# Optimization experiments

Hardware: AMD Instinct MI355X
Metric: run time of the kernel (lower is better)

Reference implementation:

```python
import jax, jax.numpy as jnp
import numpy as np

B, N, D, V = 512, 200, 128, 100000

def setup_inputs() -> dict:
    key = jax.random.key(0)
    ks = jax.random.split(key, 13)
    s = 1.0 / np.sqrt(D)
    return {
        "x": jax.random.randint(ks[0], (B, N), 0, V),
        "A": jax.random.uniform(ks[1], (B, N, 2 * N), dtype=jnp.float32),
        "emb": jax.random.normal(ks[2], (V, D), dtype=jnp.float32) * s,
        "w_in": jax.random.normal(ks[3], (D, D), dtype=jnp.float32) * s,
        "b_in": jax.random.normal(ks[4], (D,), dtype=jnp.float32) * s,
        "w_out": jax.random.normal(ks[5], (D, D), dtype=jnp.float32) * s,
        "b_out": jax.random.normal(ks[6], (D,), dtype=jnp.float32) * s,
        "w_ih": jax.random.normal(ks[7], (3 * D, 2 * D), dtype=jnp.float32) * s,
        "b_ih": jax.random.normal(ks[8], (3 * D,), dtype=jnp.float32) * s,
        "w_hh": jax.random.normal(ks[9], (3 * D, D), dtype=jnp.float32) * s,
        "b_hh": jax.random.normal(ks[10], (3 * D,), dtype=jnp.float32) * s,
        "b_iah": jax.random.normal(ks[11], (D,), dtype=jnp.float32) * s,
        "b_oah": jax.random.normal(ks[12], (D,), dtype=jnp.float32) * s,
    }

def reference(x, A, emb, w_in, b_in, w_out, b_out, w_ih, b_ih, w_hh, b_hh, b_iah, b_oah):
    hidden = emb[x]                                   # [B, N, D]
    n = A.shape[1]
    # neighbor aggregation via in/out adjacency halves
    input_in = jnp.matmul(A[:, :, :n], hidden @ w_in.T + b_in) + b_iah    # [B, N, D]
    input_out = jnp.matmul(A[:, :, n:2 * n], hidden @ w_out.T + b_out) + b_oah
    inputs = jnp.concatenate([input_in, input_out], axis=2)               # [B, N, 2D]
    gi = inputs @ w_ih.T + b_ih                        # [B, N, 3D]
    gh = hidden @ w_hh.T + b_hh                        # [B, N, 3D]
    d = hidden.shape[-1]
    i_r, i_i, i_n = gi[..., :d], gi[..., d:2 * d], gi[..., 2 * d:]
    h_r, h_i, h_n = gh[..., :d], gh[..., d:2 * d], gh[..., 2 * d:]
    gate_input = jax.nn.sigmoid(i_i + h_i)
    gate_reset = jax.nn.sigmoid(i_r + h_r)
    gate_output = jnp.tanh(i_n + gate_reset * h_n)
    return gate_output + gate_input * (hidden - gate_output)
```

## Files before the change

### kernel.cpp

```cpp
#include <hip/hip_runtime.h>
#include <math.h>

#define BB 512
#define NN 200
#define DD 128
#define BNROWS (BB*NN)

typedef float f32x4 __attribute__((ext_vector_type(4)));
typedef short bf16x8 __attribute__((ext_vector_type(8)));

#define MFMA16(a,b,c) __builtin_amdgcn_mfma_f32_16x16x32_bf16(a,b,c,0,0,0)

#define GLL(gp, lp) __builtin_amdgcn_global_load_lds( \
    (const __attribute__((address_space(1))) unsigned int*)(gp), \
    (__attribute__((address_space(3))) unsigned int*)(lp), 16, 0, 0)

#define OFF_ZHI   ((size_t)0)
#define OFF_ZLO   (OFF_ZHI + (size_t)BNROWS*384*2)
#define OFF_HT    (OFF_ZLO + (size_t)BNROWS*256*2)
#define OFF_M1    (OFF_HT  + (size_t)BB*128*224*2)
#define OFF_M2    (OFF_M1  + (size_t)384*128*4)
#define OFF_WH    (OFF_M2  + (size_t)384*128*4)
#define OFF_WL    (OFF_WH  + (size_t)512*384*2)
#define OFF_CC    (OFF_WL  + (size_t)512*384*2)
#define OFF_U1V   (OFF_CC  + 512*4)
#define OFF_U2V   (OFF_U1V + 512*4)
#define OFF_U1    (OFF_U2V + 512*4)
#define OFF_U2    (OFF_U1  + 384*4)
#define OFF_C0    (OFF_U2  + 384*4)
#define OFF_RSI   (OFF_C0  + 384*4)
#define OFF_RSO   (OFF_RSI + (size_t)BNROWS*4)
#define WS_BYTES  (OFF_RSO + (size_t)BNROWS*4)

__device__ inline unsigned short f2bf(float x) {
  unsigned int u = __float_as_uint(x);
  unsigned int r = u + 0x7FFFu + ((u >> 16) & 1u);
  return (unsigned short)(r >> 16);
}
__device__ inline float bf2f(unsigned short h) {
  return __uint_as_float(((unsigned int)h) << 16);
}
__device__ inline float fsigmoid(float x) {
  return 1.f / (1.f + __expf(-x));
}
__device__ inline float ftanh(float x) {
  x = fminf(15.f, fmaxf(-15.f, x));
  float e = __expf(-2.f * x);
  return (1.f - e) / (1.f + e);
}

__global__ __launch_bounds__(128) void kprep(
    const float* __restrict__ w_ih, const float* __restrict__ w_in,
    const float* __restrict__ w_out, const float* __restrict__ b_in,
    const float* __restrict__ b_out, const float* __restrict__ b_iah,
    const float* __restrict__ b_oah, const float* __restrict__ b_ih,
    float* __restrict__ M1, float* __restrict__ M2,
    float* __restrict__ u1, float* __restrict__ u2, float* __restrict__ c0) {
  __shared__ float wrow[256];
  const int j = blockIdx.x;
  const int k = threadIdx.x;
  wrow[k]       = w_ih[(size_t)j * 256 + k];
  wrow[128 + k] = w_ih[(size_t)j * 256 + 128 + k];
  __syncthreads();
  float a1 = 0.f, a2 = 0.f;
  for (int t = 0; t < 128; ++t) {
    a1 = fmaf(wrow[t],       w_in[t * 128 + k],  a1);
    a2 = fmaf(wrow[128 + t], w_out[t * 128 + k], a2);
  }
  M1[j * 128 + k] = a1;
  M2[j * 128 + k] = a2;
  if (k == 0) {
    float s1 = 0.f, s2 = 0.f, s0 = 0.f;
    for (int t = 0; t < 128; ++t) {
      s1 = fmaf(wrow[t], b_in[t], s1);
      s2 = fmaf(wrow[128 + t], b_out[t], s2);
      s0 = fmaf(wrow[t], b_iah[t], s0);
      s0 = fmaf(wrow[128 + t], b_oah[t], s0);
    }
    u1[j] = s1; u2[j] = s2; c0[j] = s0 + b_ih[j];
  }
}

__global__ void wcat_build(const float* __restrict__ M1, const float* __restrict__ M2,
                           const float* __restrict__ w_hh, const float* __restrict__ b_hh,
                           const float* __restrict__ u1, const float* __restrict__ u2,
                           const float* __restrict__ c0,
                           unsigned short* __restrict__ Wh, unsigned short* __restrict__ Wl,
                           float* __restrict__ cc, float* __restrict__ u1v,
                           float* __restrict__ u2v) {
  int idx = blockIdx.x * 256 + threadIdx.x;
  if (idx >= 512 * 384) return;
  int jp = idx / 384, k = idx - jp * 384;
  int nh = jp >> 8, ng = (jp >> 7) & 1, t = (jp >> 4) & 7, q = jp & 15;
  int blk = t >> 1, s = t & 1;
  int c = nh * 64 + ng * 32 + s * 16 + q;
  int g = (blk <= 1) ? blk : 2;
  int j = g * 128 + c;
  float val;
  if (k < 128)      val = (blk == 3) ? 0.f : M1[j * 128 + k];
  else if (k < 256) val = (blk == 3) ? 0.f : M2[j * 128 + (k - 128)];
  else              val = (blk == 2) ? 0.f : w_hh[(size_t)j * 128 + (k - 256)];
  unsigned short h = f2bf(val);
  Wh[idx] = h;
  Wl[idx] = f2bf(val - bf2f(h));
  if (k == 0) {
    float ccv, a1, a2;
    if (blk == 0)      { ccv = c0[c] + b_hh[c];             a1 = u1[c];       a2 = u2[c]; }
    else if (blk == 1) { ccv = c0[128 + c] + b_hh[128 + c]; a1 = u1[128 + c]; a2 = u2[128 + c]; }
    else if (blk == 2) { ccv = c0[256 + c];                 a1 = u1[256 + c]; a2 = u2[256 + c]; }
    else               { ccv = b_hh[256 + c];               a1 = 0.f;         a2 = 0.f; }
    cc[jp] = ccv; u1v[jp] = a1; u2v[jp] = a2;
  }
}

__global__ __launch_bounds__(256) void k1_gather(
    const int* __restrict__ x, const float* __restrict__ emb,
    unsigned short* __restrict__ hT, unsigned short* __restrict__ Z_hi) {
  __shared__ float hid[32][132];
  const int t = threadIdx.x;
  const int b = blockIdx.x;
  const int m0 = blockIdx.y * 32;
  for (int i = t; i < 32 * 128; i += 256) {
    int r = i >> 7, c = i & 127;
    int m = m0 + r;
    int rowc = b * 200 + (m < 200 ? m : 199);
    float h = emb[(size_t)x[rowc] * 128 + c];
    hid[r][c] = h;
    if (m < 200) Z_hi[(size_t)(b * 200 + m) * 384 + 256 + c] = f2bf(h);
  }
  __syncthreads();
  {
    int c = t >> 1, half = t & 1;
    bf16x8 p0, p1;
    #pragma unroll
    for (int j = 0; j < 16; ++j) {
      int ml = half * 16 + j;
      bool valid = (m0 + ml) < 200;
      float fv = valid ? hid[ml][c] : 0.f;
      if (j < 8) p0[j] = (short)f2bf(fv);
      else       p1[j - 8] = (short)f2bf(fv);
    }
    size_t base = ((size_t)(b * 128 + c)) * 224 + m0 + half * 16;
    *(bf16x8*)&hT[base]     = p0;
    *(bf16x8*)&hT[base + 8] = p1;
  }
}

__global__ __launch_bounds__(256) void k2_amm(
    const float* __restrict__ A, const unsigned short* __restrict__ hT,
    unsigned short* __restrict__ Z_hi, unsigned short* __restrict__ Z_lo,
    float* __restrict__ rs_in, float* __restrict__ rs_out) {
  __shared__ alignas(16) unsigned short Ainh[64][32];
  __shared__ alignas(16) unsigned short Ainl[64][32];
  __shared__ alignas(16) unsigned short Aouth[64][32];
  __shared__ alignas(16) unsigned short Aoutl[64][32];
  __shared__ alignas(16) unsigned short Bv[128][32];
  const int t = threadIdx.x;
  const int b = blockIdx.x;
  const int m0 = blockIdx.y * 64;
  const int wv_id = t >> 6, lane = t & 63;
  const int q = lane & 15, quad = lane >> 4;
  const int sel = wv_id >> 1, nh2 = wv_id & 1;
  f32x4 acc[4][4];
  #pragma unroll
  for (int i = 0; i < 4; ++i)
    #pragma unroll
    for (int j = 0; j < 4; ++j) acc[i][j] = 0.f;
  float rsi = 0.f, rso = 0.f;

  for (int k0 = 0; k0 < 224; k0 += 32) {
    __syncthreads();
    {
      int m = t >> 2, seg = t & 3;
      int gm = m0 + m, kb = k0 + seg * 8;
      float fin[8], fot[8];
      bool v = (gm < 200) && (kb < 200);
      if (v) {
        const float* arow = A + (size_t)(b * 200 + gm) * 400;
        f32x4 p0 = *(const f32x4*)(arow + kb);
        f32x4 p1 = *(const f32x4*)(arow + kb + 4);
        f32x4 q0 = *(const f32x4*)(arow + 200 + kb);
        f32x4 q1 = *(const f32x4*)(arow + 200 + kb + 4);
        fin[0]=p0.x; fin[1]=p0.y; fin[2]=p0.z; fin[3]=p0.w;
        fin[4]=p1.x; fin[5]=p1.y; fin[6]=p1.z; fin[7]=p1.w;
        fot[0]=q0.x; fot[1]=q0.y; fot[2]=q0.z; fot[3]=q0.w;
        fot[4]=q1.x; fot[5]=q1.y; fot[6]=q1.z; fot[7]=q1.w;
      } else {
        #pragma unroll
        for (int e = 0; e < 8; ++e) { fin[e] = 0.f; fot[e] = 0.f; }
      }
      bf16x8 ih, il, oh, ol;
      #pragma unroll
      for (int e = 0; e < 8; ++e) {
        rsi += fin[e]; rso += fot[e];
        unsigned short h1 = f2bf(fin[e]);
        ih[e] = (short)h1; il[e] = (short)f2bf(fin[e] - bf2f(h1));
        unsigned short h2 = f2bf(fot[e]);
        oh[e] = (short)h2; ol[e] = (short)f2bf(fot[e] - bf2f(h2));
      }
      *(bf16x8*)&Ainh[m][seg * 8]  = ih;
      *(bf16x8*)&Ainl[m][seg * 8]  = il;
      *(bf16x8*)&Aouth[m][seg * 8] = oh;
      *(bf16x8*)&Aoutl[m][seg * 8] = ol;
    }
    #pragma unroll
    for (int p = 0; p < 2; ++p) {
      int i = p * 256 + t;
      int c = i >> 2, seg = i & 3;
      size_t off = ((size_t)(b * 128 + c)) * 224 + k0 + seg * 8;
      *(bf16x8*)&Bv[c][seg * 8] = *(const bf16x8*)(hT + off);
    }
    __syncthreads();
    const unsigned short (*Ath)[32] = sel ? Aouth : Ainh;
    const unsigned short (*Atl)[32] = sel ? Aoutl : Ainl;
    bf16x8 ah[4], al[4];
    #pragma unroll
    for (int mt = 0; mt < 4; ++mt) {
      ah[mt] = *(const bf16x8*)&Ath[mt * 16 + q][quad * 8];
      al[mt] = *(const bf16x8*)&Atl[mt * 16 + q][quad * 8];
    }
    #pragma unroll
    for (int nt = 0; nt < 4; ++nt) {
      bf16x8 bb = *(const bf16x8*)&Bv[nh2 * 64 + nt * 16 + q][quad * 8];
      #pragma unroll
      for (int mt = 0; mt < 4; ++mt) {
        acc[mt][nt] = MFMA16(ah[mt], bb, acc[mt][nt]);
        acc[mt][nt] = MFMA16(al[mt], bb, acc[mt][nt]);
      }
    }
  }
  const int colbase = sel * 128;
  #pragma unroll
  for (int nt = 0; nt < 4; ++nt) {
    int c = nh2 * 64 + nt * 16 + q;
    #pragma unroll
    for (int mt = 0; mt < 4; ++mt) {
      #pragma unroll
      for (int r = 0; r < 4; ++r) {
        int m = m0 + mt * 16 + quad * 4 + r;
        if (m < 200) {
          float v = acc[mt][nt][r];
          unsigned short hs = f2bf(v);
          size_t row = (size_t)(b * 200 + m);
          Z_hi[row * 384 + colbase + c] = hs;
          Z_lo[row * 256 + colbase + c] = f2bf(v - bf2f(hs));
        }
      }
    }
  }
  rsi += __shfl_xor(rsi, 1); rsi += __shfl_xor(rsi, 2);
  rso += __shfl_xor(rso, 1); rso += __shfl_xor(rso, 2);
  {
    int m = t >> 2, gm = m0 + m;
    if ((t & 3) == 0 && gm < 200) {
      rs_in[(size_t)b * 200 + gm]  = rsi;
      rs_out[(size_t)b * 200 + gm] = rso;
    }
  }
}

__global__ __launch_bounds__(256, 2) void k3_gates(
    const unsigned short* __restrict__ Z_hi, const unsigned short* __restrict__ Z_lo,
    const unsigned short* __restrict__ Wh, const unsigned short* __restrict__ Wl,
    const float* __restrict__ cc, const float* __restrict__ u1v,
    const float* __restrict__ u2v, const float* __restrict__ rs_in,
    const float* __restrict__ rs_out, float* __restrict__ out) {
  __shared__ alignas(16) unsigned short WhS[256][32];
  __shared__ alignas(16) unsigned short WlS[256][32];
  __shared__ alignas(16) unsigned short Ah[2][128][32];
  __shared__ alignas(16) unsigned short Al[2][128][32];
  const int t = threadIdx.x;
  const int w = t >> 6, lane = t & 63;
  const int q = lane & 15, quad = lane >> 4;
  const int mh = w >> 1, ng = w & 1;
  const int lrow = lane >> 2, lseg = lane & 3;
  const size_t rbase = (size_t)blockIdx.x * 128;
  const int nh = blockIdx.y;

  f32x4 acc[4][8];
  #pragma unroll
  for (int i = 0; i < 4; ++i)
    #pragma unroll
    for (int j = 0; j < 8; ++j) acc[i][j] = 0.f;

  #define STAGE_W(KC) do {                                                      \
    const int k0_ = (KC) * 32;                                                  \
    _Pragma("unroll")                                                           \
    for (int c_ = 0; c_ < 4; ++c_) {                                            \
      int j_ = w * 64 + c_ * 16;                                                \
      GLL(Wh + (size_t)(nh * 256 + j_ + lrow) * 384 + k0_ + lseg * 8,           \
          &WhS[j_][0]);                                                         \
    }                                                                           \
    _Pragma("unroll")                                                           \
    for (int c_ = 0; c_ < 4; ++c_) {                                            \
      int j_ = w * 64 + c_ * 16;                                                \
      GLL(Wl + (size_t)(nh * 256 + j_ + lrow) * 384 + k0_ + lseg * 8,           \
          &WlS[j_][0]);                                                         \
    }                                                                           \
  } while (0)

  #define STAGE_A1(KC, BUF) do {                                                \
    const int k0_ = (KC) * 32;                                                  \
    _Pragma("unroll")                                                           \
    for (int c_ = 0; c_ < 2; ++c_) {                                            \
      int m_ = w * 32 + c_ * 16;                                                \
      GLL(Z_hi + (rbase + m_ + lrow) * 384 + k0_ + lseg * 8, &Ah[BUF][m_][0]);  \
    }                                                                           \
    _Pragma("unroll")                                                           \
    for (int c_ = 0; c_ < 2; ++c_) {                                            \
      int m_ = w * 32 + c_ * 16;                                                \
      GLL(Z_lo + (rbase + m_ + lrow) * 256 + k0_ + lseg * 8, &Al[BUF][m_][0]);  \
    }                                                                           \
  } while (0)

  #define STAGE_A2(KC, BUF) do {                                                \
    const int k0_ = (KC) * 32;                                                  \
    _Pragma("unroll")                                                           \
    for (int c_ = 0; c_ < 2; ++c_) {                                            \
      int m_ = w * 32 + c_ * 16;                                                \
      GLL(Z_hi + (rbase + m_ + lrow) * 384 + k0_ + lseg * 8, &Ah[BUF][m_][0]);  \
    }                                                                           \
  } while (0)

  #define COMPUTE1(BUF) do {                                                    \
    bf16x8 ah_[4], al_[4];                                                      \
    _Pragma("unroll")                                                           \
    for (int mt = 0; mt < 4; ++mt) {                                            \
      ah_[mt] = *(const bf16x8*)&Ah[BUF][mh * 64 + mt * 16 + q][quad * 8];      \
      al_[mt] = *(const bf16x8*)&Al[BUF][mh * 64 + mt * 16 + q][quad * 8];      \
    }                                                                           \
    _Pragma("unroll")                                                           \
    for (int tt = 0; tt < 6; ++tt) {                                            \
      bf16x8 bh = *(const bf16x8*)&WhS[ng * 128 + tt * 16 + q][quad * 8];       \
      bf16x8 bl = *(const bf16x8*)&WlS[ng * 128 + tt * 16 + q][quad * 8];       \
      _Pragma("unroll")                                                         \
      for (int mt = 0; mt < 4; ++mt) {                                          \
        acc[mt][tt] = MFMA16(ah_[mt], bh, acc[mt][tt]);                         \
        acc[mt][tt] = MFMA16(ah_[mt], bl, acc[mt][tt]);                         \
        acc[mt][tt] = MFMA16(al_[mt], bh, acc[mt][tt]);                         \
      }                                                                         \
    }                                                                           \
  } while (0)

  #define COMPUTE2(BUF) do {                                                    \
    bf16x8 ah_[4];                                                              \
    _Pragma("unroll")                                                           \
    for (int mt = 0; mt < 4; ++mt)                                              \
      ah_[mt] = *(const bf16x8*)&Ah[BUF][mh * 64 + mt * 16 + q][quad * 8];      \
    _Pragma("unroll")                                                           \
    for (int ti = 0; ti < 6; ++ti) {                                            \
      const int tt = (ti < 4) ? ti : ti + 2;             \
      bf16x8 bh = *(const bf16x8*)&WhS[ng * 128 + tt * 16 + q][quad * 8];       \
      bf16x8 bl = *(const bf16x8*)&WlS[ng * 128 + tt * 16 + q][quad * 8];       \
      _Pragma("unroll")                                                         \
      for (int mt = 0; mt < 4; ++mt) {                                          \
        acc[mt][tt] = MFMA16(ah_[mt], bh, acc[mt][tt]);                         \
        acc[mt][tt] = MFMA16(ah_[mt], bl, acc[mt][tt]);                         \
      }                                                                         \
    }                                                                           \
  } while (0)

  #define WAITV(S) asm volatile("s_waitcnt vmcnt(" S ")" ::: "memory")
  #define WAITL()  asm volatile("s_waitcnt lgkmcnt(0)" ::: "memory")
  #define BAR()    __builtin_amdgcn_s_barrier()
  #define SBAR()   __builtin_amdgcn_sched_barrier(0)

  STAGE_A1(0, 0);
  int buf = 0;
  #pragma unroll
  for (int kc = 0; kc < 7; ++kc) {
    STAGE_W(kc);
    STAGE_A1(kc + 1, buf ^ 1);
    WAITV("4"); SBAR(); BAR();
    COMPUTE1(buf);
    WAITL(); SBAR(); BAR();
    buf ^= 1;
  }
  {
    STAGE_W(7);
    STAGE_A2(8, buf ^ 1);
    WAITV("2"); SBAR(); BAR();
    COMPUTE1(buf);
    WAITL(); SBAR(); BAR();
    buf ^= 1;
  }
  #pragma unroll
  for (int kc = 8; kc < 11; ++kc) {
    STAGE_W(kc);
    STAGE_A2(kc + 1, buf ^ 1);
    WAITV("2"); SBAR(); BAR();
    COMPUTE2(buf);
    WAITL(); SBAR(); BAR();
    buf ^= 1;
  }
  {
    STAGE_W(11);
    WAITV("0"); SBAR(); BAR();
    COMPUTE2(buf);
  }

  const int jb = nh * 256 + ng * 128;
  float cs[2][4], a1s[2][3], a2s[2][3];
  #pragma unroll
  for (int s = 0; s < 2; ++s) {
    #pragma unroll
    for (int gb = 0; gb < 4; ++gb) cs[s][gb] = cc[jb + (gb * 2 + s) * 16 + q];
    #pragma unroll
    for (int gb = 0; gb < 3; ++gb) {
      a1s[s][gb] = u1v[jb + (gb * 2 + s) * 16 + q];
      a2s[s][gb] = u2v[jb + (gb * 2 + s) * 16 + q];
    }
  }
  #pragma unroll
  for (int mt = 0; mt < 4; ++mt) {
    #pragma unroll
    for (int r = 0; r < 4; ++r) {
      size_t row = rbase + mh * 64 + mt * 16 + quad * 4 + r;
      float rin = rs_in[row], rot = rs_out[row];
      #pragma unroll
      for (int s = 0; s < 2; ++s) {
        int c = nh * 64 + ng * 32 + s * 16 + q;
        float sr  = acc[mt][0 + s][r] + cs[s][0] + rin * a1s[s][0] + rot * a2s[s][0];
        float si  = acc[mt][2 + s][r] + cs[s][1] + rin * a1s[s][1] + rot * a2s[s][1];
        float ani = acc[mt][4 + s][r] + cs[s][2] + rin * a1s[s][2] + rot * a2s[s][2];
        float anh = acc[mt][6 + s][r] + cs[s][3];
        float g_rs = fsigmoid(sr);
        float g_in = fsigmoid(si);
        float g_ot = ftanh(ani + g_rs * anh);
        float h = bf2f(Z_hi[row * 384 + 256 + c]);
        out[row * 128 + c] = g_ot + g_in * (h - g_ot);
      }
    }
  }
  #undef STAGE_W
  #undef STAGE_A1
  #undef STAGE_A2
  #undef COMPUTE1
  #undef COMPUTE2
  #undef WAITV
  #undef WAITL
  #undef BAR
  #undef SBAR
}

extern "C" void kernel_launch(void* const* d_in, const int* in_sizes, int n_in,
                              void* d_out, int out_size, void* d_ws, size_t ws_size,
                              hipStream_t stream) {
  const int*   x     = (const int*)d_in[0];
  const float* A     = (const float*)d_in[1];
  const float* emb   = (const float*)d_in[2];
  const float* w_in  = (const float*)d_in[3];
  const float* b_in  = (const float*)d_in[4];
  const float* w_out = (const float*)d_in[5];
  const float* b_out = (const float*)d_in[6];
  const float* w_ih  = (const float*)d_in[7];
  const float* b_ih  = (const float*)d_in[8];
  const float* w_hh  = (const float*)d_in[9];
  const float* b_hh  = (const float*)d_in[10];
  const float* b_iah = (const float*)d_in[11];
  const float* b_oah = (const float*)d_in[12];
  float* out = (float*)d_out;
  char* ws = (char*)d_ws;

  if (ws_size < WS_BYTES) return;

  unsigned short* Z_hi = (unsigned short*)(ws + OFF_ZHI);
  unsigned short* Z_lo = (unsigned short*)(ws + OFF_ZLO);
  unsigned short* hT   = (unsigned short*)(ws + OFF_HT);
  float* M1 = (float*)(ws + OFF_M1);
  float* M2 = (float*)(ws + OFF_M2);
  unsigned short* Wh = (unsigned short*)(ws + OFF_WH);
  unsigned short* Wl = (unsigned short*)(ws + OFF_WL);
  float* ccv = (float*)(ws + OFF_CC);
  float* u1v = (float*)(ws + OFF_U1V);
  float* u2v = (float*)(ws + OFF_U2V);
  float* u1  = (float*)(ws + OFF_U1);
  float* u2  = (float*)(ws + OFF_U2);
  float* c0  = (float*)(ws + OFF_C0);
  float* rs_in  = (float*)(ws + OFF_RSI);
  float* rs_out = (float*)(ws + OFF_RSO);

  kprep<<<384, 128, 0, stream>>>(w_ih, w_in, w_out, b_in, b_out, b_iah, b_oah,
                                 b_ih, M1, M2, u1, u2, c0);
  wcat_build<<<(512 * 384 + 255) / 256, 256, 0, stream>>>(M1, M2, w_hh, b_hh,
                                                          u1, u2, c0, Wh, Wl,
                                                          ccv, u1v, u2v);
  dim3 g1(BB, 7);
  k1_gather<<<g1, 256, 0, stream>>>(x, emb, hT, Z_hi);
  dim3 g2(BB, 4);
  k2_amm<<<g2, 256, 0, stream>>>(A, hT, Z_hi, Z_lo, rs_in, rs_out);
  dim3 g3(BNROWS / 128, 2);
  k3_gates<<<g3, 256, 0, stream>>>(Z_hi, Z_lo, Wh, Wl, ccv, u1v, u2v,
                                   rs_in, rs_out, out);
}
```

Baseline: 536.3 us.

## Double-buffer k2 adjacency GEMM with register prefetch and direct-to-LDS loads

Restructures the k2_amm K-loop into a software pipeline. The next tile of A is prefetched into registers and the next tile of hT is staged straight into a second LDS buffer with global_load_lds, while the current tile is converted and multiplied. It also pads the A tiles in LDS to reduce bank conflicts and permutes hT rows so each lane can write four contiguous bf16 outputs as one vector store. Launch bounds are raised to request two blocks per CU. In exchange, the kernel uses more registers and LDS, which may limit occupancy.

```diff
diff --git a/kernel.cpp b/kernel.cpp
--- a/kernel.cpp
+++ b/kernel.cpp
@@ -8,12 +8,18 @@
 
 typedef float f32x4 __attribute__((ext_vector_type(4)));
 typedef short bf16x8 __attribute__((ext_vector_type(8)));
+typedef unsigned short u16x4 __attribute__((ext_vector_type(4)));
 
 #define MFMA16(a,b,c) __builtin_amdgcn_mfma_f32_16x16x32_bf16(a,b,c,0,0,0)
 
 #define GLL(gp, lp) __builtin_amdgcn_global_load_lds( \
     (const __attribute__((address_space(1))) unsigned int*)(gp), \
     (__attribute__((address_space(3))) unsigned int*)(lp), 16, 0, 0)
+
+#define KWAITV(S) asm volatile("s_waitcnt vmcnt(" S ")" ::: "memory")
+#define KWAITL()  asm volatile("s_waitcnt lgkmcnt(0)" ::: "memory")
+#define KBAR()    __builtin_amdgcn_s_barrier()
+#define KSBAR()   __builtin_amdgcn_sched_barrier(0)
 
 #define OFF_ZHI   ((size_t)0)
 #define OFF_ZLO   (OFF_ZHI + (size_t)BNROWS*384*2)
@@ -146,21 +152,28 @@
   }
 }
 
-__global__ __launch_bounds__(256) void k2_amm(
+__global__ __launch_bounds__(256, 2) void k2_amm(
     const float* __restrict__ A, const unsigned short* __restrict__ hT,
     unsigned short* __restrict__ Z_hi, unsigned short* __restrict__ Z_lo,
     float* __restrict__ rs_in, float* __restrict__ rs_out) {
-  __shared__ alignas(16) unsigned short Ainh[64][32];
-  __shared__ alignas(16) unsigned short Ainl[64][32];
-  __shared__ alignas(16) unsigned short Aouth[64][32];
-  __shared__ alignas(16) unsigned short Aoutl[64][32];
-  __shared__ alignas(16) unsigned short Bv[128][32];
+  __shared__ alignas(16) unsigned short Ainh[2][64][40];
+  __shared__ alignas(16) unsigned short Ainl[2][64][40];
+  __shared__ alignas(16) unsigned short Aouth[2][64][40];
+  __shared__ alignas(16) unsigned short Aoutl[2][64][40];
+  __shared__ alignas(16) unsigned short Bv[2][128][32];
   const int t = threadIdx.x;
   const int b = blockIdx.x;
   const int m0 = blockIdx.y * 64;
-  const int wv_id = t >> 6, lane = t & 63;
+  const int wv = t >> 6, lane = t & 63;
   const int q = lane & 15, quad = lane >> 4;
-  const int sel = wv_id >> 1, nh2 = wv_id & 1;
+  const int sel = wv >> 1, nh2 = wv & 1;
+  const int lrow = lane >> 2, lseg = lane & 3;
+
+  const int am = t >> 2, aseg = t & 3;
+  const int gm = m0 + am;
+  const bool mvalid = gm < 200;
+  const float* arow = A + (size_t)(b * 200 + (mvalid ? gm : 199)) * 400;
+
   f32x4 acc[4][4];
   #pragma unroll
   for (int i = 0; i < 4; ++i)
@@ -168,95 +181,123 @@
     for (int j = 0; j < 4; ++j) acc[i][j] = 0.f;
   float rsi = 0.f, rso = 0.f;
 
-  for (int k0 = 0; k0 < 224; k0 += 32) {
-    __syncthreads();
-    {
-      int m = t >> 2, seg = t & 3;
-      int gm = m0 + m, kb = k0 + seg * 8;
-      float fin[8], fot[8];
-      bool v = (gm < 200) && (kb < 200);
-      if (v) {
-        const float* arow = A + (size_t)(b * 200 + gm) * 400;
-        f32x4 p0 = *(const f32x4*)(arow + kb);
-        f32x4 p1 = *(const f32x4*)(arow + kb + 4);
-        f32x4 q0 = *(const f32x4*)(arow + 200 + kb);
-        f32x4 q1 = *(const f32x4*)(arow + 200 + kb + 4);
-        fin[0]=p0.x; fin[1]=p0.y; fin[2]=p0.z; fin[3]=p0.w;
-        fin[4]=p1.x; fin[5]=p1.y; fin[6]=p1.z; fin[7]=p1.w;
-        fot[0]=q0.x; fot[1]=q0.y; fot[2]=q0.z; fot[3]=q0.w;
-        fot[4]=q1.x; fot[5]=q1.y; fot[6]=q1.z; fot[7]=q1.w;
-      } else {
+  #define AISSUE(K0, P0, P1, Q0, Q1) do {                                       \
+    int kb_ = (K0) + aseg * 8;                                                  \
+    int kc_ = (kb_ < 200) ? kb_ : 0;                                            \
+    P0 = *(const f32x4*)(arow + kc_);                                           \
+    P1 = *(const f32x4*)(arow + kc_ + 4);                                       \
+    Q0 = *(const f32x4*)(arow + 200 + kc_);                                     \
+    Q1 = *(const f32x4*)(arow + 200 + kc_ + 4);                                 \
+  } while (0)
+
+  #define STAGE_B(K0, BUF) do {                                                 \
+    _Pragma("unroll")                                                           \
+    for (int op_ = 0; op_ < 2; ++op_) {                                         \
+      int j_ = wv * 32 + op_ * 16 + lrow;                                       \
+      int c_ = ((j_ >> 6) << 6) + ((j_ & 15) << 2) + ((j_ >> 4) & 3);           \
+      GLL(hT + ((size_t)(b * 128 + c_)) * 224 + (K0) + lseg * 8,                \
+          &Bv[BUF][wv * 32 + op_ * 16][0]);                                     \
+    }                                                                           \
+  } while (0)
+
+  #define ACONV(K0, BUF, P0, P1, Q0, Q1) do {                                   \
+    bool kv_ = mvalid && ((K0) + aseg * 8 < 200);                               \
+    float fin_[8], fot_[8];                                                     \
+    fin_[0]=P0.x; fin_[1]=P0.y; fin_[2]=P0.z; fin_[3]=P0.w;                     \
+    fin_[4]=P1.x; fin_[5]=P1.y; fin_[6]=P1.z; fin_[7]=P1.w;                     \
+    fot_[0]=Q0.x; fot_[1]=Q0.y; fot_[2]=Q0.z; fot_[3]=Q0.w;                     \
+    fot_[4]=Q1.x; fot_[5]=Q1.y; fot_[6]=Q1.z; fot_[7]=Q1.w;                     \
+    bf16x8 ih_, il_, oh_, ol_;                                                  \
+    _Pragma("unroll")                                                           \
+    for (int e_ = 0; e_ < 8; ++e_) {                                            \
+      float fi_ = kv_ ? fin_[e_] : 0.f;                                         \
+      float fo_ = kv_ ? fot_[e_] : 0.f;                                         \
+      rsi += fi_; rso += fo_;                                                   \
+      unsigned short h1_ = f2bf(fi_);                                           \
+      ih_[e_] = (short)h1_; il_[e_] = (short)f2bf(fi_ - bf2f(h1_));             \
+      unsigned short h2_ = f2bf(fo_);                                           \
+      oh_[e_] = (short)h2_; ol_[e_] = (short)f2bf(fo_ - bf2f(h2_));             \
+    }                                                                           \
+    *(bf16x8*)&Ainh[BUF][am][aseg * 8]  = ih_;                                  \
+    *(bf16x8*)&Ainl[BUF][am][aseg * 8]  = il_;                                  \
+    *(bf16x8*)&Aouth[BUF][am][aseg * 8] = oh_;                                  \
+    *(bf16x8*)&Aoutl[BUF][am][aseg * 8] = ol_;                                  \
+  } while (0)
+
+  #define K2COMP(BUF) do {                                                      \
+    const unsigned short (*Ath_)[40] = sel ? Aouth[BUF] : Ainh[BUF];            \
+    const unsigned short (*Atl_)[40] = sel ? Aoutl[BUF] : Ainl[BUF];            \
+    bf16x8 ah_[4], al_[4];                                                      \
+    _Pragma("unroll")                                                           \
+    for (int mt = 0; mt < 4; ++mt) {                                            \
+      ah_[mt] = *(const bf16x8*)&Ath_[mt * 16 + q][quad * 8];                   \
+      al_[mt] = *(const bf16x8*)&Atl_[mt * 16 + q][quad * 8];                   \
+    }                                                                           \
+    _Pragma("unroll")                                                           \
+    for (int nt = 0; nt < 4; ++nt) {                                            \
+      bf16x8 bb_ = *(const bf16x8*)&Bv[BUF][nh2 * 64 + nt * 16 + q][quad * 8];  \
+      _Pragma("unroll")                                                         \
+      for (int mt = 0; mt < 4; ++mt) {                                          \
+        acc[mt][nt] = MFMA16(ah_[mt], bb_, acc[mt][nt]);                        \
+        acc[mt][nt] = MFMA16(al_[mt], bb_, acc[mt][nt]);                        \
+      }                                                                         \
+    }                                                                           \
+  } while (0)
+
+  f32x4 cp0, cp1, cq0, cq1;
+  AISSUE(0, cp0, cp1, cq0, cq1);
+  STAGE_B(0, 0);
+  int buf = 0;
+
+  for (int k = 0; k < 6; ++k) {
+    const int k0n = (k + 1) * 32;
+    f32x4 np0, np1, nq0, nq1;
+    AISSUE(k0n, np0, np1, nq0, nq1);
+    STAGE_B(k0n, buf ^ 1);
+    KWAITV("6"); KSBAR();
+    ACONV(k * 32, buf, cp0, cp1, cq0, cq1);
+    KWAITL(); KSBAR(); KBAR();
+    K2COMP(buf);
+    KBAR();
+    cp0 = np0; cp1 = np1; cq0 = nq0; cq1 = nq1;
+    buf ^= 1;
+  }
+  KWAITV("0"); KSBAR();
+  ACONV(192, buf, cp0, cp1, cq0, cq1);
+  KWAITL(); KSBAR(); KBAR();
+  K2COMP(buf);
+
+  const int colb = sel * 128 + nh2 * 64 + q * 4;
+  #pragma unroll
+  for (int mt = 0; mt < 4; ++mt) {
+    #pragma unroll
+    for (int r = 0; r < 4; ++r) {
+      int m = m0 + mt * 16 + quad * 4 + r;
+      if (m < 200) {
+        u16x4 h4, l4;
         #pragma unroll
-        for (int e = 0; e < 8; ++e) { fin[e] = 0.f; fot[e] = 0.f; }
-      }
-      bf16x8 ih, il, oh, ol;
-      #pragma unroll
-      for (int e = 0; e < 8; ++e) {
-        rsi += fin[e]; rso += fot[e];
-        unsigned short h1 = f2bf(fin[e]);
-        ih[e] = (short)h1; il[e] = (short)f2bf(fin[e] - bf2f(h1));
-        unsigned short h2 = f2bf(fot[e]);
-        oh[e] = (short)h2; ol[e] = (short)f2bf(fot[e] - bf2f(h2));
-      }
-      *(bf16x8*)&Ainh[m][seg * 8]  = ih;
-      *(bf16x8*)&Ainl[m][seg * 8]  = il;
-      *(bf16x8*)&Aouth[m][seg * 8] = oh;
-      *(bf16x8*)&Aoutl[m][seg * 8] = ol;
-    }
-    #pragma unroll
-    for (int p = 0; p < 2; ++p) {
-      int i = p * 256 + t;
-      int c = i >> 2, seg = i & 3;
-      size_t off = ((size_t)(b * 128 + c)) * 224 + k0 + seg * 8;
-      *(bf16x8*)&Bv[c][seg * 8] = *(const bf16x8*)(hT + off);
-    }
-    __syncthreads();
-    const unsigned short (*Ath)[32] = sel ? Aouth : Ainh;
-    const unsigned short (*Atl)[32] = sel ? Aoutl : Ainl;
-    bf16x8 ah[4], al[4];
-    #pragma unroll
-    for (int mt = 0; mt < 4; ++mt) {
-      ah[mt] = *(const bf16x8*)&Ath[mt * 16 + q][quad * 8];
-      al[mt] = *(const bf16x8*)&Atl[mt * 16 + q][quad * 8];
-    }
-    #pragma unroll
-    for (int nt = 0; nt < 4; ++nt) {
-      bf16x8 bb = *(const bf16x8*)&Bv[nh2 * 64 + nt * 16 + q][quad * 8];
-      #pragma unroll
-      for (int mt = 0; mt < 4; ++mt) {
-        acc[mt][nt] = MFMA16(ah[mt], bb, acc[mt][nt]);
-        acc[mt][nt] = MFMA16(al[mt], bb, acc[mt][nt]);
+        for (int nt = 0; nt < 4; ++nt) {
+          float v = acc[mt][nt][r];
+          unsigned short hs = f2bf(v);
+          h4[nt] = hs;
+          l4[nt] = f2bf(v - bf2f(hs));
+        }
+        size_t row = (size_t)(b * 200 + m);
+        *(u16x4*)&Z_hi[row * 384 + colb] = h4;
+        *(u16x4*)&Z_lo[row * 256 + colb] = l4;
       }
     }
   }
-  const int colbase = sel * 128;
-  #pragma unroll
-  for (int nt = 0; nt < 4; ++nt) {
-    int c = nh2 * 64 + nt * 16 + q;
-    #pragma unroll
-    for (int mt = 0; mt < 4; ++mt) {
-      #pragma unroll
-      for (int r = 0; r < 4; ++r) {
-        int m = m0 + mt * 16 + quad * 4 + r;
-        if (m < 200) {
-          float v = acc[mt][nt][r];
-          unsigned short hs = f2bf(v);
-          size_t row = (size_t)(b * 200 + m);
-          Z_hi[row * 384 + colbase + c] = hs;
-          Z_lo[row * 256 + colbase + c] = f2bf(v - bf2f(hs));
-        }
-      }
-    }
-  }
   rsi += __shfl_xor(rsi, 1); rsi += __shfl_xor(rsi, 2);
   rso += __shfl_xor(rso, 1); rso += __shfl_xor(rso, 2);
-  {
-    int m = t >> 2, gm = m0 + m;
-    if ((t & 3) == 0 && gm < 200) {
-      rs_in[(size_t)b * 200 + gm]  = rsi;
-      rs_out[(size_t)b * 200 + gm] = rso;
-    }
-  }
+  if (aseg == 0 && mvalid) {
+    rs_in[(size_t)b * 200 + gm]  = rsi;
+    rs_out[(size_t)b * 200 + gm] = rso;
+  }
+  #undef AISSUE
+  #undef STAGE_B
+  #undef ACONV
+  #undef K2COMP
 }
 
 __global__ __launch_bounds__(256, 2) void k3_gates(
@@ -360,42 +401,37 @@
     }                                                                           \
   } while (0)
 
-  #define WAITV(S) asm volatile("s_waitcnt vmcnt(" S ")" ::: "memory")
-  #define WAITL()  asm volatile("s_waitcnt lgkmcnt(0)" ::: "memory")
-  #define BAR()    __builtin_amdgcn_s_barrier()
-  #define SBAR()   __builtin_amdgcn_sched_barrier(0)
-
   STAGE_A1(0, 0);
   int buf = 0;
   #pragma unroll
   for (int kc = 0; kc < 7; ++kc) {
     STAGE_W(kc);
     STAGE_A1(kc + 1, buf ^ 1);
-    WAITV("4"); SBAR(); BAR();
+    KWAITV("4"); KSBAR(); KBAR();
     COMPUTE1(buf);
-    WAITL(); SBAR(); BAR();
+    KWAITL(); KSBAR(); KBAR();
     buf ^= 1;
   }
   {
     STAGE_W(7);
     STAGE_A2(8, buf ^ 1);
-    WAITV("2"); SBAR(); BAR();
+    KWAITV("2"); KSBAR(); KBAR();
     COMPUTE1(buf);
-    WAITL(); SBAR(); BAR();
+    KWAITL(); KSBAR(); KBAR();
     buf ^= 1;
   }
   #pragma unroll
   for (int kc = 8; kc < 11; ++kc) {
     STAGE_W(kc);
     STAGE_A2(kc + 1, buf ^ 1);
-    WAITV("2"); SBAR(); BAR();
+    KWAITV("2"); KSBAR(); KBAR();
     COMPUTE2(buf);
-    WAITL(); SBAR(); BAR();
+    KWAITL(); KSBAR(); KBAR();
     buf ^= 1;
   }
   {
     STAGE_W(11);
-    WAITV("0"); SBAR(); BAR();
+    KWAITV("0"); KSBAR(); KBAR();
     COMPUTE2(buf);
   }
 
@@ -437,10 +473,6 @@
   #undef STAGE_A2
   #undef COMPUTE1
   #undef COMPUTE2
-  #undef WAITV
-  #undef WAITL
-  #undef BAR
-  #undef SBAR
 }
 
 extern "C" void kernel_launch(void* const* d_in, const int* in_sizes, int n_in,
```

Result: faster. 503.9 us (-6.0%).
